# Performance work log

Measured on AMD Instinct MI355X. Metric: run time of the kernel, lower is better.

Reference implementation:

```python
import jax, jax.numpy as jnp
from jax import lax
import numpy as np

EPS = 1e-6
LOG_STD_MIN = -20.0
LOG_STD_MAX = 2.0


def _leaky(x):
    return jnp.where(x >= 0, x, 0.01 * x)


def _conv(x, w, b):
    # x: [B,C,H,W], w: [O,C,3,3] -> VALID conv, NCHW
    y = lax.conv_general_dilated(x, w, (1, 1), 'VALID',
                                 dimension_numbers=('NCHW', 'OIHW', 'NCHW'))
    return y + b[None, :, None, None]


def _gru_last(seq, Wih, Whh, bih, bhh):
    # seq: [B,T,In]; PyTorch GRU cell semantics, h0 = 0. Returns h_T: [B,H]
    B = seq.shape[0]
    H = Whh.shape[1]
    h0 = jnp.zeros((B, H), seq.dtype)

    def step(h, x_t):
        gi = x_t @ Wih.T + bih          # [B,3H]
        gh = h @ Whh.T + bhh            # [B,3H]
        i_r, i_z, i_n = jnp.split(gi, 3, axis=-1)
        h_r, h_z, h_n = jnp.split(gh, 3, axis=-1)
        r = jax.nn.sigmoid(i_r + h_r)
        z = jax.nn.sigmoid(i_z + h_z)
        n = jnp.tanh(i_n + r * h_n)
        h_new = (1.0 - z) * n + z * h
        return h_new, None

    h_last, _ = lax.scan(step, h0, jnp.swapaxes(seq, 0, 1))
    return h_last


def setup_inputs() -> dict:
    key = jax.random.key(0)
    ks = jax.random.split(key, 16)
    B, C, T, S = 4096, 3, 64, 128   # batch, in_channels, window, num_stocks
    H = S + 1                        # GRU hidden / action dim = 129
    In = S - 4                       # GRU input size = 124

    def w_init(k, shape, fan_in):
        return jax.random.normal(k, shape, jnp.float32) * np.sqrt(2.0 / fan_in).astype(np.float32)

    inp = {
        'x': jax.random.normal(ks[0], (B, C, T, S), jnp.float32),
        'w': jax.random.uniform(ks[1], (B, H), jnp.float32),
        'eps': jax.random.normal(ks[2], (B, H), jnp.float32),
        'conv1_w': w_init(ks[3], (2 * C, C, 3, 3), C * 9),
        'conv1_b': jnp.zeros((2 * C,), jnp.float32),
        'conv2_w': w_init(ks[4], (1, 2 * C, 3, 3), 2 * C * 9),
        'conv2_b': jnp.zeros((1,), jnp.float32),
        'gru_Wih': w_init(ks[5], (3 * H, In), In),
        'gru_Whh': w_init(ks[6], (3 * H, H), H),
        'gru_bih': jnp.zeros((3 * H,), jnp.float32),
        'gru_bhh': jnp.zeros((3 * H,), jnp.float32),
        'fc_mu_w': w_init(ks[7], (H, 2 * H), 2 * H),
        'fc_mu_b': jnp.zeros((H,), jnp.float32),
        'fc_ls_w': w_init(ks[8], (H, 2 * H), 2 * H),
        'fc_ls_b': jnp.zeros((H,), jnp.float32),
    }
    return inp


def reference(x, w, eps, conv1_w, conv1_b, conv2_w, conv2_b,
              gru_Wih, gru_Whh, gru_bih, gru_bhh,
              fc_mu_w, fc_mu_b, fc_ls_w, fc_ls_b):
    h = _leaky(_conv(x, conv1_w, conv1_b))            # [B,2C,T-2,S-2]
    h = _leaky(_conv(h, conv2_w, conv2_b))            # [B,1,T-4,S-4]
    seq = jnp.squeeze(h, axis=1)                      # [B,T-4,S-4]
    g = _leaky(_gru_last(seq, gru_Wih, gru_Whh, gru_bih, gru_bhh))  # [B,H]
    feat = jnp.concatenate([g, w], axis=-1)           # [B,2H]
    mu = feat @ fc_mu_w.T + fc_mu_b                   # [B,H]
    log_std = jnp.clip(feat @ fc_ls_w.T + fc_ls_b, LOG_STD_MIN, LOG_STD_MAX)
    std = jnp.exp(log_std)
    # Normal.sample() is detached in torch -> stop_gradient
    xs = lax.stop_gradient(mu + std * eps)
    pi_action = jnp.tanh(xs)
    # Normal.log_prob(xs) - log(1 - tanh(xs)^2 + EPS)
    log_pi = (-0.5 * jnp.square((xs - mu) / std) - log_std
              - 0.5 * jnp.log(2.0 * jnp.pi).astype(xs.dtype)
              - jnp.log(1.0 - jnp.square(pi_action) + EPS))
    log_pi = jnp.sum(log_pi, axis=-1, keepdims=True)  # [B,1]
    pi_action = pi_action + 1.0
    pi_action = pi_action / jnp.sum(pi_action, axis=-1, keepdims=True)
    return pi_action, log_pi
```

## Files before the change

kernel.cpp:

```cpp
#include <hip/hip_runtime.h>
#include <math.h>

#define BTOT   4096
#define CIN    3
#define TIN    64
#define SIN    128

#define SEQ_OFF    0
#define G_OFF      (SEQ_OFF + 4096*60*124)
#define HST_OFF    (G_OFF + 4096*129)
#define AWHH_OFF   (HST_OFF + 4096*132)
#define AWIH_OFF   (AWHH_OFF + 64000)
#define MUWP_OFF   (AWIH_OFF + 51200)
#define LSWP_OFF   (MUWP_OFF + 129*260)
#define GIC_OFF    (LSWP_OFF + 129*260)

typedef __attribute__((ext_vector_type(8))) short bf16x8;
typedef __attribute__((ext_vector_type(4))) float f32x4;

__device__ __forceinline__ float fast_tanh(float x) {
    float ax = fabsf(x);
    float t  = __expf(-2.f * ax);
    float r  = (1.f - t) / (1.f + t);
    return copysignf(r, x);
}
__device__ __forceinline__ float fast_sigmoid(float x) {
    return 1.f / (1.f + __expf(-x));
}
__device__ __forceinline__ unsigned short f2bf(float x) {
    unsigned int u = __float_as_uint(x);
    unsigned int r = u + 0x7FFFu + ((u >> 16) & 1u);
    return (unsigned short)(r >> 16);
}
__device__ __forceinline__ float bf2f(unsigned short b) {
    return __uint_as_float(((unsigned int)b) << 16);
}

__global__ __launch_bounds__(256) void prep_pad(
    const float* __restrict__ Whh, const float* __restrict__ Wih,
    const float* __restrict__ muw, const float* __restrict__ lsw,
    float* __restrict__ ws)
{
    int idx = blockIdx.x * 256 + threadIdx.x;
    const int NHH = 25 * 5 * 2 * 512;
    const int NIA = 25 * 4 * 2 * 512;
    const int N2  = 129 * 260;
    if (idx < NHH) {
        int a      = idx;
        int frag   = a >> 9;
        int within = a & 511;
        int l      = within >> 3;
        int c      = within & 7;
        int half   = frag & 1;
        int q      = frag >> 1;
        int kt     = q % 5;
        int jt     = q / 5;
        int j      = jt * 16 + (l & 15);
        int k      = kt * 32 + (l >> 4) * 8 + c;
        float v    = (j < 387 && k < 129) ? Whh[(size_t)j * 129 + k] : 0.f;
        unsigned short hb = f2bf(v);
        ((short*)(ws + AWHH_OFF))[a] = (short)((half == 0) ? hb : f2bf(v - bf2f(hb)));
    } else if (idx < NHH + NIA) {
        int a      = idx - NHH;
        int frag   = a >> 9;
        int within = a & 511;
        int l      = within >> 3;
        int c      = within & 7;
        int half   = frag & 1;
        int q      = frag >> 1;
        int kt     = q & 3;
        int jt     = q >> 2;
        int j      = jt * 16 + (l & 15);
        int k      = kt * 32 + (l >> 4) * 8 + c;
        float v    = (j < 387 && k < 124) ? Wih[(size_t)j * 124 + k] : 0.f;
        unsigned short hb = f2bf(v);
        ((short*)(ws + AWIH_OFF))[a] = (short)((half == 0) ? hb : f2bf(v - bf2f(hb)));
    } else if (idx < NHH + NIA + N2) {
        int i = idx - NHH - NIA; int j = i / 260, k = i - j * 260;
        ws[MUWP_OFF + i] = (k < 258) ? muw[j * 258 + k] : 0.f;
    } else if (idx < NHH + NIA + 2 * N2) {
        int i = idx - NHH - NIA - N2; int j = i / 260, k = i - j * 260;
        ws[LSWP_OFF + i] = (k < 258) ? lsw[j * 258 + k] : 0.f;
    }
}

#define RACC(F4_, F2_, W0_, W1_, W2_) \
    acc0 += (F4_).x*(W0_) + (F4_).y*(W1_) + (F4_).z*(W2_); \
    acc1 += (F4_).y*(W0_) + (F4_).z*(W1_) + (F4_).w*(W2_); \
    acc2 += (F4_).z*(W0_) + (F4_).w*(W1_) + (F2_).x*(W2_); \
    acc3 += (F4_).w*(W0_) + (F2_).x*(W1_) + (F2_).y*(W2_);

#define LDSET(S, TR_) { \
    S##0_4 = *(const float4*)(xc0 + (TR_) * 128 + s0); \
    S##0_2 = *(const float2*)(xc0 + (TR_) * 128 + f2c); \
    S##1_4 = *(const float4*)(xc1 + (TR_) * 128 + s0); \
    S##1_2 = *(const float2*)(xc1 + (TR_) * 128 + f2c); \
    S##2_4 = *(const float4*)(xc2 + (TR_) * 128 + s0); \
    S##2_2 = *(const float2*)(xc2 + (TR_) * 128 + f2c); }

#define C1STEP(SA, SB, SC, TQ_) { \
    float acc0 = bo, acc1 = bo, acc2 = bo, acc3 = bo; \
    RACC(SA##0_4, SA##0_2, w000, w001, w002) \
    RACC(SA##1_4, SA##1_2, w100, w101, w102) \
    RACC(SA##2_4, SA##2_2, w200, w201, w202) \
    RACC(SB##0_4, SB##0_2, w010, w011, w012) \
    RACC(SB##1_4, SB##1_2, w110, w111, w112) \
    RACC(SB##2_4, SB##2_2, w210, w211, w212) \
    RACC(SC##0_4, SC##0_2, w020, w021, w022) \
    RACC(SC##1_4, SC##1_2, w120, w121, w122) \
    RACC(SC##2_4, SC##2_2, w220, w221, w222) \
    float4 r_; \
    r_.x = (acc0 >= 0.f) ? acc0 : 0.01f * acc0; \
    r_.y = (acc1 >= 0.f) ? acc1 : 0.01f * acc1; \
    r_.z = (acc2 >= 0.f) ? acc2 : 0.01f * acc2; \
    r_.w = (acc3 >= 0.f) ? acc3 : 0.01f * acc3; \
    *(float4*)(h1t + (o * 12 + (TQ_)) * 128 + s0) = r_; }

#define C2SEG(o_, kt_, W0_, W1_, W2_) { \
    const float* rp_ = h1t + ((o_) * 12 + tq + (kt_)) * 128 + s0; \
    float4 v4_ = *(const float4*)rp_; \
    float2 v2_ = *(const float2*)(rp_ + 4); \
    acc0 += v4_.x*(W0_) + v4_.y*(W1_) + v4_.z*(W2_); \
    acc1 += v4_.y*(W0_) + v4_.z*(W1_) + v4_.w*(W2_); \
    acc2 += v4_.z*(W0_) + v4_.w*(W1_) + v2_.x*(W2_); \
    acc3 += v4_.w*(W0_) + v2_.x*(W1_) + v2_.y*(W2_); }

__global__ __launch_bounds__(256) void conv_fused(
    const float* __restrict__ x,
    const float* __restrict__ w1, const float* __restrict__ b1,
    const float* __restrict__ w2, const float* __restrict__ b2,
    float* __restrict__ seq)
{
    __shared__ __attribute__((aligned(16))) float h1t[6 * 12 * 128];
    __shared__ float w1s[162];
    __shared__ float w2s[54];
    __shared__ float b1s[6];
    __shared__ float b2s;

    const int tid  = threadIdx.x;
    const int tile = blockIdx.x;
    const int bb   = blockIdx.y;
    const int T0   = tile * 10;

    if (tid < 162)                  w1s[tid] = w1[tid];
    if (tid >= 192 && tid < 246)    w2s[tid - 192] = w2[tid - 192];
    if (tid >= 248 && tid < 254)    b1s[tid - 248] = b1[tid - 248];
    if (tid == 255)                 b2s = b2[0];
    __syncthreads();

    if (tid < 192) {
        const int o   = tid >> 5;
        const int s0  = (tid & 31) * 4;
        const int f2c = (s0 < 124) ? (s0 + 4) : 122;
        const float* wb = w1s + o * 27;
        float w000 = wb[0],  w001 = wb[1],  w002 = wb[2];
        float w010 = wb[3],  w011 = wb[4],  w012 = wb[5];
        float w020 = wb[6],  w021 = wb[7],  w022 = wb[8];
        float w100 = wb[9],  w101 = wb[10], w102 = wb[11];
        float w110 = wb[12], w111 = wb[13], w112 = wb[14];
        float w120 = wb[15], w121 = wb[16], w122 = wb[17];
        float w200 = wb[18], w201 = wb[19], w202 = wb[20];
        float w210 = wb[21], w211 = wb[22], w212 = wb[23];
        float w220 = wb[24], w221 = wb[25], w222 = wb[26];
        float bo = b1s[o];

        const float* xc0 = x + (size_t)bb * (3 * 64 * 128) + (size_t)T0 * 128;
        const float* xc1 = xc0 + 64 * 128;
        const float* xc2 = xc0 + 2 * 64 * 128;

        float4 A0_4, A1_4, A2_4, B0_4, B1_4, B2_4, C0_4, C1_4, C2_4;
        float2 A0_2, A1_2, A2_2, B0_2, B1_2, B2_2, C0_2, C1_2, C2_2;

        LDSET(A, 0)
        LDSET(B, 1)
        LDSET(C, 2)  C1STEP(A, B, C, 0)
        LDSET(A, 3)  C1STEP(B, C, A, 1)
        LDSET(B, 4)  C1STEP(C, A, B, 2)
        LDSET(C, 5)  C1STEP(A, B, C, 3)
        LDSET(A, 6)  C1STEP(B, C, A, 4)
        LDSET(B, 7)  C1STEP(C, A, B, 5)
        LDSET(C, 8)  C1STEP(A, B, C, 6)
        LDSET(A, 9)  C1STEP(B, C, A, 7)
        LDSET(B, 10) C1STEP(C, A, B, 8)
        LDSET(C, 11) C1STEP(A, B, C, 9)
        LDSET(A, 12) C1STEP(B, C, A, 10)
        LDSET(B, 13) C1STEP(C, A, B, 11)
    }
    __syncthreads();

    {
        float u000 = w2s[0],  u001 = w2s[1],  u002 = w2s[2];
        float u010 = w2s[3],  u011 = w2s[4],  u012 = w2s[5];
        float u020 = w2s[6],  u021 = w2s[7],  u022 = w2s[8];
        float u100 = w2s[9],  u101 = w2s[10], u102 = w2s[11];
        float u110 = w2s[12], u111 = w2s[13], u112 = w2s[14];
        float u120 = w2s[15], u121 = w2s[16], u122 = w2s[17];
        float u200 = w2s[18], u201 = w2s[19], u202 = w2s[20];
        float u210 = w2s[21], u211 = w2s[22], u212 = w2s[23];
        float u220 = w2s[24], u221 = w2s[25], u222 = w2s[26];
        float u300 = w2s[27], u301 = w2s[28], u302 = w2s[29];
        float u310 = w2s[30], u311 = w2s[31], u312 = w2s[32];
        float u320 = w2s[33], u321 = w2s[34], u322 = w2s[35];
        float u400 = w2s[36], u401 = w2s[37], u402 = w2s[38];
        float u410 = w2s[39], u411 = w2s[40], u412 = w2s[41];
        float u420 = w2s[42], u421 = w2s[43], u422 = w2s[44];
        float u500 = w2s[45], u501 = w2s[46], u502 = w2s[47];
        float u510 = w2s[48], u511 = w2s[49], u512 = w2s[50];
        float u520 = w2s[51], u521 = w2s[52], u522 = w2s[53];
        float bo2 = b2s;
        for (int idx = tid; idx < 310; idx += 256) {
            const int tq = idx / 31;
            const int s0 = (idx - tq * 31) * 4;
            float acc0 = bo2, acc1 = bo2, acc2 = bo2, acc3 = bo2;
            C2SEG(0, 0, u000, u001, u002)
            C2SEG(0, 1, u010, u011, u012)
            C2SEG(0, 2, u020, u021, u022)
            C2SEG(1, 0, u100, u101, u102)
            C2SEG(1, 1, u110, u111, u112)
            C2SEG(1, 2, u120, u121, u122)
            C2SEG(2, 0, u200, u201, u202)
            C2SEG(2, 1, u210, u211, u212)
            C2SEG(2, 2, u220, u221, u222)
            C2SEG(3, 0, u300, u301, u302)
            C2SEG(3, 1, u310, u311, u312)
            C2SEG(3, 2, u320, u321, u322)
            C2SEG(4, 0, u400, u401, u402)
            C2SEG(4, 1, u410, u411, u412)
            C2SEG(4, 2, u420, u421, u422)
            C2SEG(5, 0, u500, u501, u502)
            C2SEG(5, 1, u510, u511, u512)
            C2SEG(5, 2, u520, u521, u522)
            float4 r;
            r.x = (acc0 >= 0.f) ? acc0 : 0.01f * acc0;
            r.y = (acc1 >= 0.f) ? acc1 : 0.01f * acc1;
            r.z = (acc2 >= 0.f) ? acc2 : 0.01f * acc2;
            r.w = (acc3 >= 0.f) ? acc3 : 0.01f * acc3;
            *(float4*)(seq + ((size_t)bb * 60 + T0 + tq) * 124 + s0) = r;
        }
    }
}

__global__ __launch_bounds__(512) void gi_mfma(
    const float* __restrict__ seq, const short* __restrict__ awih,
    float* __restrict__ gic, int t0, int nt)
{
    __shared__ __attribute__((aligned(16))) short Bs[4 * 2 * 128 * 5 * 8];

    const int tid = threadIdx.x;
    const int l   = tid & 63;
    const int w   = tid >> 6;
    const int jt  = blockIdx.y;
    const int b0  = blockIdx.x * 128;

    const bf16x8* at = (const bf16x8*)awih;
    const int abase = jt * 8 * 64 + l;
    bf16x8 Ah0 = at[abase + 0 * 128];
    bf16x8 Al0 = at[abase + 0 * 128 + 64];
    bf16x8 Ah1 = at[abase + 1 * 128];
    bf16x8 Al1 = at[abase + 1 * 128 + 64];
    bf16x8 Ah2 = at[abase + 2 * 128];
    bf16x8 Al2 = at[abase + 2 * 128 + 64];
    bf16x8 Ah3 = at[abase + 3 * 128];
    bf16x8 Al3 = at[abase + 3 * 128 + 64];

    if (tid < 128) {
        *(unsigned long long*)(Bs + ((6 * 128 + tid) * 5 + 3) * 8 + 4) = 0ull;
        *(unsigned long long*)(Bs + ((7 * 128 + tid) * 5 + 3) * 8 + 4) = 0ull;
    }
    __syncthreads();

    for (int tt = 0; tt < nt; ++tt) {
        const int t = t0 + tt;
        for (int f = tid; f < 3968; f += 512) {
            int bi = f / 31;
            int kf = f - bi * 31;
            float4 v = *(const float4*)(seq + ((size_t)(b0 + bi) * 60 + t) * 124 + kf * 4);
            int k0   = kf * 4;
            int kt   = k0 >> 5;
            int ksub = (k0 >> 3) & 3;
            int c0   = k0 & 7;
            unsigned short h0 = f2bf(v.x), h1 = f2bf(v.y), h2 = f2bf(v.z), h3 = f2bf(v.w);
            unsigned short l0 = f2bf(v.x - bf2f(h0));
            unsigned short l1 = f2bf(v.y - bf2f(h1));
            unsigned short l2 = f2bf(v.z - bf2f(h2));
            unsigned short l3 = f2bf(v.w - bf2f(h3));
            unsigned long long hp = (unsigned long long)h0 | ((unsigned long long)h1 << 16)
                                  | ((unsigned long long)h2 << 32) | ((unsigned long long)h3 << 48);
            unsigned long long lp = (unsigned long long)l0 | ((unsigned long long)l1 << 16)
                                  | ((unsigned long long)l2 << 32) | ((unsigned long long)l3 << 48);
            *(unsigned long long*)(Bs + (((kt * 2 + 0) * 128 + bi) * 5 + ksub) * 8 + c0) = hp;
            *(unsigned long long*)(Bs + (((kt * 2 + 1) * 128 + bi) * 5 + ksub) * 8 + c0) = lp;
        }
        __syncthreads();

        f32x4 acc = {0.f, 0.f, 0.f, 0.f};
        const int bn   = w * 16 + (l & 15);
        const int ksub = l >> 4;
        #define GI_KT(KT, AH, AL) { \
            bf16x8 bh = *(const bf16x8*)(Bs + ((((KT) * 2 + 0) * 128 + bn) * 5 + ksub) * 8); \
            bf16x8 bl = *(const bf16x8*)(Bs + ((((KT) * 2 + 1) * 128 + bn) * 5 + ksub) * 8); \
            acc = __builtin_amdgcn_mfma_f32_16x16x32_bf16(AL, bh, acc, 0, 0, 0); \
            acc = __builtin_amdgcn_mfma_f32_16x16x32_bf16(AH, bl, acc, 0, 0, 0); \
            acc = __builtin_amdgcn_mfma_f32_16x16x32_bf16(AH, bh, acc, 0, 0, 0); }
        GI_KT(0, Ah0, Al0)
        GI_KT(1, Ah1, Al1)
        GI_KT(2, Ah2, Al2)
        GI_KT(3, Ah3, Al3)
        #undef GI_KT

        {
            float* gt = gic + (size_t)tt * 387 * 4096;
            int row0 = (l >> 4) * 4;
            #pragma unroll
            for (int i = 0; i < 4; ++i) {
                int j = jt * 16 + row0 + i;
                if (j < 387)
                    gt[(size_t)j * 4096 + b0 + bn] = acc[i];
            }
        }
        __syncthreads();
    }
}

__global__ __launch_bounds__(512) void gru_mfma(
    const float* __restrict__ gic, const short* __restrict__ awhh,
    const float* __restrict__ bih, const float* __restrict__ bhh,
    float* __restrict__ hstate, float* __restrict__ g_out,
    int t0, int nt)
{
    __shared__ __attribute__((aligned(16))) short hbf[2 * 16 * 168];
    __shared__ float hs2[16 * 132];
    __shared__ float GHb[16 * 390];
    __shared__ float bihS[387];
    __shared__ float bhhS[387];

    const int tid  = threadIdx.x;
    const int l    = tid & 63;
    const int w    = tid >> 6;
    const int b0   = blockIdx.x * 16;
    const int bcol = l & 15;
    const int krow = l >> 4;

    if (tid < 387) { bihS[tid] = bih[tid]; bhhS[tid] = bhh[tid]; }
    for (int e = tid; e < 2688; e += 512) ((unsigned int*)hbf)[e] = 0u;
    if (t0 == 0) {
        for (int e = tid; e < 16 * 132; e += 512) hs2[e] = 0.f;
        __syncthreads();
    } else {
        for (int e = tid; e < 16 * 132; e += 512) hs2[e] = hstate[(size_t)b0 * 132 + e];
        __syncthreads();
        for (int e = tid; e < 2064; e += 512) {
            int r = e & 15, j = e >> 4;
            float v = hs2[r * 132 + j];
            unsigned short hb = f2bf(v);
            hbf[r * 168 + j]        = (short)hb;
            hbf[2688 + r * 168 + j] = (short)f2bf(v - bf2f(hb));
        }
        __syncthreads();
    }

    const bf16x8* at = (const bf16x8*)awhh;

    #define GATE(E, PGA, PGB, PGC) { \
        int r_ = (E) & 15, j_ = (E) >> 4; \
        float pr_  = (PGA) + GHb[r_ * 390 + j_]       + bihS[j_]       + bhhS[j_]; \
        float pz_  = (PGB) + GHb[r_ * 390 + 129 + j_] + bihS[129 + j_] + bhhS[129 + j_]; \
        float gin_ = (PGC) + bihS[258 + j_]; \
        float ghn_ = GHb[r_ * 390 + 258 + j_] + bhhS[258 + j_]; \
        float rg_ = fast_sigmoid(pr_); \
        float zg_ = fast_sigmoid(pz_); \
        float nn_ = fast_tanh(gin_ + rg_ * ghn_); \
        float hn_ = (1.f - zg_) * nn_ + zg_ * hs2[r_ * 132 + j_]; \
        hs2[r_ * 132 + j_] = hn_; \
        unsigned short hb_ = f2bf(hn_); \
        hbf[r_ * 168 + j_]        = (short)hb_; \
        hbf[2688 + r_ * 168 + j_] = (short)f2bf(hn_ - bf2f(hb_)); }

    for (int tt = 0; tt < nt; ++tt) {
        const float* gib = gic + (size_t)tt * 387 * 4096 + b0;
        float pa0, pb0, pc0, pa1, pb1, pc1, pa2, pb2, pc2, pa3, pb3, pc3;
        {
            int r = tid & 15, j = tid >> 4;
            pa0 = gib[(size_t)j * 4096 + r];
            pb0 = gib[(size_t)(129 + j) * 4096 + r];
            pc0 = gib[(size_t)(258 + j) * 4096 + r];
            int e = tid + 512; r = e & 15; j = e >> 4;
            pa1 = gib[(size_t)j * 4096 + r];
            pb1 = gib[(size_t)(129 + j) * 4096 + r];
            pc1 = gib[(size_t)(258 + j) * 4096 + r];
            e = tid + 1024; r = e & 15; j = e >> 4;
            pa2 = gib[(size_t)j * 4096 + r];
            pb2 = gib[(size_t)(129 + j) * 4096 + r];
            pc2 = gib[(size_t)(258 + j) * 4096 + r];
            e = tid + 1536; r = e & 15; j = e >> 4;
            pa3 = gib[(size_t)j * 4096 + r];
            pb3 = gib[(size_t)(129 + j) * 4096 + r];
            pc3 = gib[(size_t)(258 + j) * 4096 + r];
        }

        f32x4 acc0 = {0.f,0.f,0.f,0.f}, acc1 = {0.f,0.f,0.f,0.f};
        f32x4 acc2 = {0.f,0.f,0.f,0.f}, acc3 = {0.f,0.f,0.f,0.f};
        #pragma unroll
        for (int kt = 0; kt < 5; ++kt) {
            bf16x8 bh = *(const bf16x8*)(hbf + bcol * 168 + kt * 32 + krow * 8);
            bf16x8 bl = *(const bf16x8*)(hbf + 2688 + bcol * 168 + kt * 32 + krow * 8);
            {
                int fb = ((w * 5 + kt) * 2) * 64 + l;
                bf16x8 Ah = at[fb], Al = at[fb + 64];
                acc0 = __builtin_amdgcn_mfma_f32_16x16x32_bf16(Al, bh, acc0, 0, 0, 0);
                acc0 = __builtin_amdgcn_mfma_f32_16x16x32_bf16(Ah, bl, acc0, 0, 0, 0);
                acc0 = __builtin_amdgcn_mfma_f32_16x16x32_bf16(Ah, bh, acc0, 0, 0, 0);
            }
            {
                int fb = (((8 + w) * 5 + kt) * 2) * 64 + l;
                bf16x8 Ah = at[fb], Al = at[fb + 64];
                acc1 = __builtin_amdgcn_mfma_f32_16x16x32_bf16(Al, bh, acc1, 0, 0, 0);
                acc1 = __builtin_amdgcn_mfma_f32_16x16x32_bf16(Ah, bl, acc1, 0, 0, 0);
                acc1 = __builtin_amdgcn_mfma_f32_16x16x32_bf16(Ah, bh, acc1, 0, 0, 0);
            }
            {
                int fb = (((16 + w) * 5 + kt) * 2) * 64 + l;
                bf16x8 Ah = at[fb], Al = at[fb + 64];
                acc2 = __builtin_amdgcn_mfma_f32_16x16x32_bf16(Al, bh, acc2, 0, 0, 0);
                acc2 = __builtin_amdgcn_mfma_f32_16x16x32_bf16(Ah, bl, acc2, 0, 0, 0);
                acc2 = __builtin_amdgcn_mfma_f32_16x16x32_bf16(Ah, bh, acc2, 0, 0, 0);
            }
            if (w == 0) {
                int fb = ((24 * 5 + kt) * 2) * 64 + l;
                bf16x8 Ah = at[fb], Al = at[fb + 64];
                acc3 = __builtin_amdgcn_mfma_f32_16x16x32_bf16(Al, bh, acc3, 0, 0, 0);
                acc3 = __builtin_amdgcn_mfma_f32_16x16x32_bf16(Ah, bl, acc3, 0, 0, 0);
                acc3 = __builtin_amdgcn_mfma_f32_16x16x32_bf16(Ah, bh, acc3, 0, 0, 0);
            }
        }
        {
            int rb = bcol * 390;
            int j0 = w * 16 + krow * 4;
            GHb[rb + j0 + 0] = acc0[0];
            GHb[rb + j0 + 1] = acc0[1];
            GHb[rb + j0 + 2] = acc0[2];
            GHb[rb + j0 + 3] = acc0[3];
            int j1 = (8 + w) * 16 + krow * 4;
            GHb[rb + j1 + 0] = acc1[0];
            GHb[rb + j1 + 1] = acc1[1];
            GHb[rb + j1 + 2] = acc1[2];
            GHb[rb + j1 + 3] = acc1[3];
            int j2 = (16 + w) * 16 + krow * 4;
            GHb[rb + j2 + 0] = acc2[0];
            GHb[rb + j2 + 1] = acc2[1];
            GHb[rb + j2 + 2] = acc2[2];
            GHb[rb + j2 + 3] = acc2[3];
            if (w == 0 && krow == 0) {
                GHb[rb + 384] = acc3[0];
                GHb[rb + 385] = acc3[1];
                GHb[rb + 386] = acc3[2];
            }
        }
        __syncthreads();

        GATE(tid,        pa0, pb0, pc0)
        GATE(tid + 512,  pa1, pb1, pc1)
        GATE(tid + 1024, pa2, pb2, pc2)
        GATE(tid + 1536, pa3, pb3, pc3)
        if (tid < 16) {
            float ta = gib[(size_t)128 * 4096 + tid];
            float tb = gib[(size_t)257 * 4096 + tid];
            float tc = gib[(size_t)386 * 4096 + tid];
            GATE(2048 + tid, ta, tb, tc)
        }
        __syncthreads();
    }

    for (int e = tid; e < 16 * 132; e += 512) hstate[(size_t)b0 * 132 + e] = hs2[e];
    if (t0 + nt >= 60) {
        for (int e = tid; e < 2064; e += 512) {
            int r = e & 15, j = e >> 4;
            float v = hs2[r * 132 + j];
            g_out[(size_t)(b0 + r) * 129 + j] = (v >= 0.f) ? v : 0.01f * v;
        }
        if (tid < 16) {
            float v = hs2[tid * 132 + 128];
            g_out[(size_t)(b0 + tid) * 129 + 128] = (v >= 0.f) ? v : 0.01f * v;
        }
    }
    #undef GATE
}

__global__ __launch_bounds__(256) void head_kernel(
    const float* __restrict__ gbuf, const float* __restrict__ wvec,
    const float* __restrict__ eps,
    const float* __restrict__ muwp, const float* __restrict__ lswp,
    const float* __restrict__ mub,  const float* __restrict__ lsb,
    float* __restrict__ out)
{
    __shared__ __attribute__((aligned(16))) float feat[16 * 260];
    __shared__ float PA[16 * 130];
    __shared__ float TERM[16 * 130];
    __shared__ float ROWSUM[16];
    __shared__ float ROWLOG[16];

    const int tid = threadIdx.x;
    const int b0  = blockIdx.x * 16;

    for (int i = tid; i < 16 * 260; i += 256) {
        int r = i / 260;
        int k = i - r * 260;
        float v = 0.f;
        if (k < 129)       v = gbuf[(size_t)(b0 + r) * 129 + k];
        else if (k < 258)  v = wvec[(size_t)(b0 + r) * 129 + (k - 129)];
        feat[i] = v;
    }
    __syncthreads();

    for (int idx = tid; idx < 16 * 129; idx += 256) {
        int r = idx & 15;
        int j = idx >> 4;
        const float4* fv = (const float4*)(feat + r * 260);
        const float4* mw = (const float4*)(muwp + (size_t)j * 260);
        const float4* lw = (const float4*)(lswp + (size_t)j * 260);
        float am = 0.f, al = 0.f;
        for (int k = 0; k < 65; ++k) {
            float4 f = fv[k];
            float4 m = mw[k];
            float4 l = lw[k];
            am += f.x * m.x + f.y * m.y + f.z * m.z + f.w * m.w;
            al += f.x * l.x + f.y * l.y + f.z * l.z + f.w * l.w;
        }
        float mu = am + mub[j];
        float ls = fminf(fmaxf(al + lsb[j], -20.f), 2.f);
        float sd = __expf(ls);
        float e  = eps[(size_t)(b0 + r) * 129 + j];
        float xv = mu + sd * e;
        float pa = fast_tanh(xv);
        float tt = (xv - mu) / sd;
        float term = -0.5f * tt * tt - ls - 0.91893853320467274f
                     - __logf(1.f - pa * pa + 1e-6f);
        PA[r * 130 + j]   = pa;
        TERM[r * 130 + j] = term;
    }
    __syncthreads();

    {
        int r = tid >> 4;
        int i = tid & 15;
        float sp = 0.f, st = 0.f;
        for (int j = i; j < 129; j += 16) {
            sp += PA[r * 130 + j];
            st += TERM[r * 130 + j];
        }
        for (int off = 8; off > 0; off >>= 1) {
            sp += __shfl_down(sp, off, 16);
            st += __shfl_down(st, off, 16);
        }
        if (i == 0) { ROWSUM[r] = sp + 129.f; ROWLOG[r] = st; }
    }
    __syncthreads();

    for (int idx = tid; idx < 16 * 129; idx += 256) {
        int r = idx & 15;
        int j = idx >> 4;
        out[(size_t)(b0 + r) * 129 + j] = (PA[r * 130 + j] + 1.f) / ROWSUM[r];
    }
    if (tid < 16)
        out[(size_t)4096 * 129 + b0 + tid] = ROWLOG[tid];
}

extern "C" void kernel_launch(void* const* d_in, const int* in_sizes, int n_in,
                              void* d_out, int out_size, void* d_ws, size_t ws_size,
                              hipStream_t stream)
{
    const float* x   = (const float*)d_in[0];
    const float* wv  = (const float*)d_in[1];
    const float* eps = (const float*)d_in[2];
    const float* c1w = (const float*)d_in[3];
    const float* c1b = (const float*)d_in[4];
    const float* c2w = (const float*)d_in[5];
    const float* c2b = (const float*)d_in[6];
    const float* Wih = (const float*)d_in[7];
    const float* Whh = (const float*)d_in[8];
    const float* bih = (const float*)d_in[9];
    const float* bhh = (const float*)d_in[10];
    const float* muw = (const float*)d_in[11];
    const float* mub = (const float*)d_in[12];
    const float* lsw = (const float*)d_in[13];
    const float* lsb = (const float*)d_in[14];

    float* ws     = (float*)d_ws;
    float* seq    = ws + SEQ_OFF;
    float* g      = ws + G_OFF;
    float* hstate = ws + HST_OFF;
    const short* awhh = (const short*)(ws + AWHH_OFF);
    const short* awih = (const short*)(ws + AWIH_OFF);
    float* muwp   = ws + MUWP_OFF;
    float* lswp   = ws + LSWP_OFF;
    float* gic    = ws + GIC_OFF;
    float* outp   = (float*)d_out;

    const long per_t = 387L * 4096;
    long avail = (long)(ws_size / 4) - (long)GIC_OFF;
    int CT = 60;
    if (avail < 60 * per_t) {
        CT = (int)(avail / per_t);
        if (CT < 1) CT = 1;
        if (CT > 60) CT = 60;
    }

    const int prep_elems = 25 * 5 * 2 * 512 + 25 * 4 * 2 * 512 + 2 * (129 * 260);
    prep_pad<<<(prep_elems + 255) / 256, 256, 0, stream>>>(Whh, Wih, muw, lsw, ws);
    conv_fused<<<dim3(6, BTOT), 256, 0, stream>>>(x, c1w, c1b, c2w, c2b, seq);

    for (int t0 = 0; t0 < 60; t0 += CT) {
        int nt = 60 - t0; if (nt > CT) nt = CT;
        gi_mfma<<<dim3(32, 25), 512, 0, stream>>>(seq, awih, gic, t0, nt);
        gru_mfma<<<256, 512, 0, stream>>>(gic, awhh, bih, bhh, hstate, g, t0, nt);
    }
    head_kernel<<<BTOT / 16, 256, 0, stream>>>(g, wv, eps, muwp, lswp, mub, lsb, outp);
}
```

Before: 1.642 ms.

## Precompute bf16 hi/lo split of seq once instead of per gi block

Adds a seq2bf kernel that converts the GRU input sequence into packed bf16 hi/lo fragments in the MFMA operand layout, written to a global buffer. gi_mfma then reads B fragments directly from global memory and no longer stages them in shared memory, which removes its LDS writes and barriers. The goal is to stop each of the 25 jt blocks from repeating the same fp32-to-bf16 conversion. The cost is an extra kernel launch plus a new global buffer that is written and read back, and that buffer shrinks the chunk size CT when workspace is tight.

```diff
diff --git a/kernel.cpp b/kernel.cpp
--- a/kernel.cpp
+++ b/kernel.cpp
@@ -13,7 +13,11 @@
 #define AWIH_OFF   (AWHH_OFF + 64000)
 #define MUWP_OFF   (AWIH_OFF + 51200)
 #define LSWP_OFF   (MUWP_OFF + 129*260)
-#define GIC_OFF    (LSWP_OFF + 129*260)
+#define BUF_OFF    (LSWP_OFF + 129*260)
+
+#define PER_T_GIC   (387 * 4096)
+#define PER_T_SBF   655360
+#define SBF_T_SH    1310720
 
 typedef __attribute__((ext_vector_type(8))) short bf16x8;
 typedef __attribute__((ext_vector_type(4))) float f32x4;
@@ -240,17 +244,53 @@
     }
 }
 
+__global__ __launch_bounds__(256) void seq2bf(
+    const float* __restrict__ seq, unsigned long long* __restrict__ sbf,
+    int t0, int nt)
+{
+    long a = (long)blockIdx.x * 256 + threadIdx.x;
+    if (a >= (long)nt * 327680) return;
+    int tt  = (int)(a / 327680);
+    int u   = (int)(a - (long)tt * 327680);
+    int chunk = u / 10240;
+    int q   = u - chunk * 10240;
+    int c0  = (q & 1) * 4;  q >>= 1;
+    int ksub = q % 5;       q /= 5;
+    int bi  = q & 127;
+    int frag = q >> 7;
+    int half = frag & 1;
+    int kt   = frag >> 1;
+    int k0   = kt * 32 + ksub * 8 + c0;
+
+    unsigned long long outp = 0ull;
+    if (ksub < 4 && k0 < 124) {
+        float4 v = *(const float4*)(seq +
+            ((size_t)(chunk * 128 + bi) * 60 + (t0 + tt)) * 124 + k0);
+        unsigned short s0, s1, s2, s3;
+        if (half == 0) {
+            s0 = f2bf(v.x); s1 = f2bf(v.y); s2 = f2bf(v.z); s3 = f2bf(v.w);
+        } else {
+            s0 = f2bf(v.x - bf2f(f2bf(v.x)));
+            s1 = f2bf(v.y - bf2f(f2bf(v.y)));
+            s2 = f2bf(v.z - bf2f(f2bf(v.z)));
+            s3 = f2bf(v.w - bf2f(f2bf(v.w)));
+        }
+        outp = (unsigned long long)s0 | ((unsigned long long)s1 << 16)
+             | ((unsigned long long)s2 << 32) | ((unsigned long long)s3 << 48);
+    }
+    sbf[a] = outp;
+}
+
 __global__ __launch_bounds__(512) void gi_mfma(
-    const float* __restrict__ seq, const short* __restrict__ awih,
-    float* __restrict__ gic, int t0, int nt)
+    const short* __restrict__ sbf, const short* __restrict__ awih,
+    float* __restrict__ gic, int nt)
 {
-    __shared__ __attribute__((aligned(16))) short Bs[4 * 2 * 128 * 5 * 8];
-
     const int tid = threadIdx.x;
     const int l   = tid & 63;
     const int w   = tid >> 6;
     const int jt  = blockIdx.y;
-    const int b0  = blockIdx.x * 128;
+    const int bx  = blockIdx.x;
+    const int b0  = bx * 128;
 
     const bf16x8* at = (const bf16x8*)awih;
     const int abase = jt * 8 * 64 + l;
@@ -263,42 +303,17 @@
     bf16x8 Ah3 = at[abase + 3 * 128];
     bf16x8 Al3 = at[abase + 3 * 128 + 64];
 
-    if (tid < 128) {
-        *(unsigned long long*)(Bs + ((6 * 128 + tid) * 5 + 3) * 8 + 4) = 0ull;
-        *(unsigned long long*)(Bs + ((7 * 128 + tid) * 5 + 3) * 8 + 4) = 0ull;
-    }
-    __syncthreads();
+    const int bn   = w * 16 + (l & 15);
+    const int ksub = l >> 4;
+    const int off0 = bx * 40960 + (bn * 5 + ksub) * 8;
+    const int row0 = ksub * 4;
 
     for (int tt = 0; tt < nt; ++tt) {
-        const int t = t0 + tt;
-        for (int f = tid; f < 3968; f += 512) {
-            int bi = f / 31;
-            int kf = f - bi * 31;
-            float4 v = *(const float4*)(seq + ((size_t)(b0 + bi) * 60 + t) * 124 + kf * 4);
-            int k0   = kf * 4;
-            int kt   = k0 >> 5;
-            int ksub = (k0 >> 3) & 3;
-            int c0   = k0 & 7;
-            unsigned short h0 = f2bf(v.x), h1 = f2bf(v.y), h2 = f2bf(v.z), h3 = f2bf(v.w);
-            unsigned short l0 = f2bf(v.x - bf2f(h0));
-            unsigned short l1 = f2bf(v.y - bf2f(h1));
-            unsigned short l2 = f2bf(v.z - bf2f(h2));
-            unsigned short l3 = f2bf(v.w - bf2f(h3));
-            unsigned long long hp = (unsigned long long)h0 | ((unsigned long long)h1 << 16)
-                                  | ((unsigned long long)h2 << 32) | ((unsigned long long)h3 << 48);
-            unsigned long long lp = (unsigned long long)l0 | ((unsigned long long)l1 << 16)
-                                  | ((unsigned long long)l2 << 32) | ((unsigned long long)l3 << 48);
-            *(unsigned long long*)(Bs + (((kt * 2 + 0) * 128 + bi) * 5 + ksub) * 8 + c0) = hp;
-            *(unsigned long long*)(Bs + (((kt * 2 + 1) * 128 + bi) * 5 + ksub) * 8 + c0) = lp;
-        }
-        __syncthreads();
-
+        const short* sb = sbf + (size_t)tt * SBF_T_SH + off0;
         f32x4 acc = {0.f, 0.f, 0.f, 0.f};
-        const int bn   = w * 16 + (l & 15);
-        const int ksub = l >> 4;
         #define GI_KT(KT, AH, AL) { \
-            bf16x8 bh = *(const bf16x8*)(Bs + ((((KT) * 2 + 0) * 128 + bn) * 5 + ksub) * 8); \
-            bf16x8 bl = *(const bf16x8*)(Bs + ((((KT) * 2 + 1) * 128 + bn) * 5 + ksub) * 8); \
+            bf16x8 bh = *(const bf16x8*)(sb + ((KT) * 2 + 0) * 5120); \
+            bf16x8 bl = *(const bf16x8*)(sb + ((KT) * 2 + 1) * 5120); \
             acc = __builtin_amdgcn_mfma_f32_16x16x32_bf16(AL, bh, acc, 0, 0, 0); \
             acc = __builtin_amdgcn_mfma_f32_16x16x32_bf16(AH, bl, acc, 0, 0, 0); \
             acc = __builtin_amdgcn_mfma_f32_16x16x32_bf16(AH, bh, acc, 0, 0, 0); }
@@ -308,17 +323,13 @@
         GI_KT(3, Ah3, Al3)
         #undef GI_KT
 
-        {
-            float* gt = gic + (size_t)tt * 387 * 4096;
-            int row0 = (l >> 4) * 4;
-            #pragma unroll
-            for (int i = 0; i < 4; ++i) {
-                int j = jt * 16 + row0 + i;
-                if (j < 387)
-                    gt[(size_t)j * 4096 + b0 + bn] = acc[i];
-            }
-        }
-        __syncthreads();
+        float* gt = gic + (size_t)tt * 387 * 4096;
+        #pragma unroll
+        for (int i = 0; i < 4; ++i) {
+            int j = jt * 16 + row0 + i;
+            if (j < 387)
+                gt[(size_t)j * 4096 + b0 + bn] = acc[i];
+        }
     }
 }
 
@@ -593,17 +604,18 @@
     const short* awih = (const short*)(ws + AWIH_OFF);
     float* muwp   = ws + MUWP_OFF;
     float* lswp   = ws + LSWP_OFF;
-    float* gic    = ws + GIC_OFF;
     float* outp   = (float*)d_out;
 
-    const long per_t = 387L * 4096;
-    long avail = (long)(ws_size / 4) - (long)GIC_OFF;
+    const long per_t = (long)PER_T_GIC + PER_T_SBF;
+    long avail = (long)(ws_size / 4) - (long)BUF_OFF;
     int CT = 60;
     if (avail < 60 * per_t) {
         CT = (int)(avail / per_t);
         if (CT < 1) CT = 1;
         if (CT > 60) CT = 60;
     }
+    float* sbff = ws + BUF_OFF;
+    float* gic  = ws + BUF_OFF + (size_t)CT * PER_T_SBF;
 
     const int prep_elems = 25 * 5 * 2 * 512 + 25 * 4 * 2 * 512 + 2 * (129 * 260);
     prep_pad<<<(prep_elems + 255) / 256, 256, 0, stream>>>(Whh, Wih, muw, lsw, ws);
@@ -611,7 +623,9 @@
 
     for (int t0 = 0; t0 < 60; t0 += CT) {
         int nt = 60 - t0; if (nt > CT) nt = CT;
-        gi_mfma<<<dim3(32, 25), 512, 0, stream>>>(seq, awih, gic, t0, nt);
+        long nb = ((long)nt * 327680 + 255) / 256;
+        seq2bf<<<(int)nb, 256, 0, stream>>>(seq, (unsigned long long*)sbff, t0, nt);
+        gi_mfma<<<dim3(32, 25), 512, 0, stream>>>((const short*)sbff, awih, gic, nt);
         gru_mfma<<<256, 512, 0, stream>>>(gic, awhh, bih, bhh, hstate, g, t0, nt);
     }
     head_kernel<<<BTOT / 16, 256, 0, stream>>>(g, wv, eps, muwp, lswp, mub, lsb, outp);
```

Result: faster. 1.510 ms, median of 2 (-8.0%).
